# Kernel optimization log

Measured on AMD Instinct MI355X. Metric: run time of the kernel, lower is better.

The kernel has to match this reference:

```python
import jax, jax.numpy as jnp
import numpy as np

DIMS = 1024
HEAD = 16
HEAD_DIM = DIMS // HEAD
MAX_ITERS = 3
THRESH = 0.01   # torch uses self.threshold.item() -> plain float, no grad
FACTOR = 0.1    # torch uses self.factor.item()
EPS = 1e-5


def _ln(x, w):
    # LayerNorm(bias=False): (x-mean)/sqrt(var+eps) * w
    m = jnp.mean(x, axis=-1, keepdims=True)
    xc = x - m
    v = jnp.mean(xc * xc, axis=-1, keepdims=True)
    return xc * jax.lax.rsqrt(v + EPS) * w


def _focus(xw, Wq, bq, Wk, Wv, bv, Wo, bo, lna_w, lnb_w,
           lq_w, lq_b, lk_w, lk_b, lv_w, lv_b):
    # xw: [B, S, DIMS]. NOTE: in the torch code xa is effectively ignored inside
    # create_qkv (k/v are computed from x due to the `xa is not None` branch bug),
    # so each window is pure self-attention on the query window.
    B, S, D = xw.shape
    xn = _ln(xw, lna_w)
    scale = HEAD_DIM ** -0.25
    q = (xn @ Wq.T + bq) * scale
    k = (xn @ Wk.T) * scale          # k Linear has no bias
    v = xn @ Wv.T + bv

    def shp(t):
        return t.reshape(B, S, HEAD, HEAD_DIM).transpose(0, 2, 1, 3)  # [B,h,S,d]

    q, k, v = shp(q), shp(k), shp(v)
    q = _ln(q, lnb_w)
    k = _ln(k, lnb_w)

    causal = jnp.tril(jnp.ones((S, S), dtype=bool))
    neg = jnp.finfo(jnp.float32).min
    inv_sqrt_d = 1.0 / np.sqrt(HEAD_DIM).astype(np.float32)

    q_cur = q
    prev = jnp.zeros_like(q)
    attn_out = jnp.zeros_like(q)
    done = jnp.array(False)

    # eff_span == S here (span_len >= win_size, ctx % win_size == 0), so the
    # [:eff_span] slices in torch are no-ops. Unrolled loop with where-gating
    # reproduces the data-dependent early exit and stays reverse-differentiable.
    for it in range(MAX_ITERS):
        qp = _ln(q_cur @ lq_w.T + lq_b, lnb_w)
        kp = _ln(k @ lk_w.T + lk_b, lnb_w)
        vp = v @ lv_w.T + lv_b
        s = jnp.einsum('bhqd,bhkd->bhqk', qp, kp) * inv_sqrt_d
        s = jnp.where(causal, s, neg)
        a = jax.nn.softmax(s, axis=-1)
        o = jnp.einsum('bhqk,bhkd->bhqd', a, vp)
        # torch: permute(0,2,1,3).flatten(2) -> [B,S,h*d], then (buggy) raw
        # view(B, HEAD, S, HEAD_DIM) with NO transpose; out_proj is NOT applied
        # in this branch. Reproduced faithfully.
        iter_out = (o.transpose(0, 2, 1, 3)
                     .reshape(B, S, HEAD * HEAD_DIM)
                     .reshape(B, HEAD, S, HEAD_DIM))
        diff = jnp.mean(jnp.abs(iter_out - prev))
        conv = jnp.logical_and(diff < THRESH + FACTOR * diff, it > 0)
        attn_out = jnp.where(done, attn_out, iter_out)
        upd = jnp.logical_or(done, conv)
        q_cur = jnp.where(upd, q_cur, q_cur + iter_out)
        prev = jnp.where(upd, prev, iter_out)
        done = upd

    out = attn_out.transpose(0, 2, 1, 3).reshape(B, S, D)
    return out @ Wo.T + bo


def setup_inputs() -> dict:
    key = jax.random.key(0)
    ks = jax.random.split(key, 10)

    def w(k, shape, s=0.02):
        return jax.random.normal(k, shape, dtype=jnp.float32) * s

    return {
        'x': jax.random.normal(ks[0], (4, 4096, DIMS), dtype=jnp.float32),
        'Wq': w(ks[1], (DIMS, DIMS)), 'bq': jnp.zeros((DIMS,), jnp.float32),
        'Wk': w(ks[2], (DIMS, DIMS)),
        'Wv': w(ks[3], (DIMS, DIMS)), 'bv': jnp.zeros((DIMS,), jnp.float32),
        'Wo': w(ks[4], (DIMS, DIMS)), 'bo': jnp.zeros((DIMS,), jnp.float32),
        'lna_w': jnp.ones((DIMS,), jnp.float32),
        'lnb_w': jnp.ones((HEAD_DIM,), jnp.float32),
        'lq_w': w(ks[5], (HEAD_DIM, HEAD_DIM), 0.1), 'lq_b': jnp.zeros((HEAD_DIM,), jnp.float32),
        'lk_w': w(ks[6], (HEAD_DIM, HEAD_DIM), 0.1), 'lk_b': jnp.zeros((HEAD_DIM,), jnp.float32),
        'lv_w': w(ks[7], (HEAD_DIM, HEAD_DIM), 0.1), 'lv_b': jnp.zeros((HEAD_DIM,), jnp.float32),
        'win_size': 512,
        'span_len': 1024,
    }


def reference(x, Wq, bq, Wk, Wv, bv, Wo, bo, lna_w, lnb_w,
              lq_w, lq_b, lk_w, lk_b, lv_w, lv_b, win_size, span_len):
    # span_len only influences eff_span in torch; with span_len >= win_size it
    # has no effect on the math (k/v come from the query window due to the bug).
    b, ctx, dims = x.shape
    nwin = ctx // win_size  # ctx chosen divisible by win_size
    xw = x.reshape(b, nwin, win_size, dims).transpose(1, 0, 2, 3)  # [nwin,B,W,D]
    f = lambda xx: _focus(xx, Wq, bq, Wk, Wv, bv, Wo, bo, lna_w, lnb_w,
                          lq_w, lq_b, lk_w, lk_b, lv_w, lv_b)
    out = jax.vmap(f)(xw)  # per-window convergence test, matching torch
    return out.transpose(1, 0, 2, 3).reshape(b, ctx, dims)
```

## Files before the change

kernel.cpp:

```cpp
#include <hip/hip_runtime.h>
#include <math.h>

#define DIMS   1024
#define NHEAD  16
#define HD     64
#define WIN    512
#define CTX    4096
#define NBATCH 4
#define NROWS  (NBATCH*CTX)
#define NUNITS (NROWS*NHEAD)
#define LNEPS  1e-5f
#define FIXSCALE 16777216.0

typedef __attribute__((ext_vector_type(8))) short bf16x8;
typedef __attribute__((ext_vector_type(4))) float f32x4;

__device__ __forceinline__ float4 ld4(const float* p) { return *reinterpret_cast<const float4*>(p); }
__device__ __forceinline__ void st4(float* p, float4 v) { *reinterpret_cast<float4*>(p) = v; }

__device__ __forceinline__ float wave_sum64(float v) {
#pragma unroll
    for (int off = 32; off; off >>= 1) v += __shfl_xor(v, off, 64);
    return v;
}
__device__ __forceinline__ float grp16_sum(float v) {
    v += __shfl_xor(v, 1, 64);
    v += __shfl_xor(v, 2, 64);
    v += __shfl_xor(v, 4, 64);
    v += __shfl_xor(v, 8, 64);
    return v;
}

__device__ __forceinline__ unsigned bf16_rn_bits(float x) {
    unsigned u = __float_as_uint(x);
    return (u + 0x7fffu + ((u >> 16) & 1u)) >> 16;
}
__device__ __forceinline__ unsigned pack_hl(float x) {
    unsigned h = bf16_rn_bits(x);
    float hf = __uint_as_float(h << 16);
    unsigned l = bf16_rn_bits(x - hf);
    return (h << 16) | (l & 0xffffu);
}

__device__ __forceinline__ unsigned cvtpk_bf16(float a, float b) {
    unsigned r;
    asm volatile("v_cvt_pk_bf16_f32 %0, %1, %2" : "=v"(r) : "v"(a), "v"(b));
    return r;
}
__device__ __forceinline__ void split_pair(float a, float b, unsigned& hw, unsigned& lw) {
    hw = cvtpk_bf16(a, b);
    float ha = __uint_as_float(hw << 16);
    float hb = __uint_as_float(hw & 0xffff0000u);
    lw = cvtpk_bf16(a - ha, b - hb);
}

__device__ __forceinline__ int swzo(int row, int kbyte) {
    return ((row << 7) + kbyte) ^ ((row & 7) << 4);
}

__global__ __launch_bounds__(256)
void ln1024_pack_kernel(const float* __restrict__ x, const float* __restrict__ w,
                        unsigned* __restrict__ outp) {
    int r = blockIdx.x;
    int tid = threadIdx.x;
    const float* xr = x + (size_t)r * DIMS;
    float4 v = ld4(xr + (tid << 2));
    __shared__ float red[8];
    float s = wave_sum64(v.x + v.y + v.z + v.w);
    int wv = tid >> 6, lane = tid & 63;
    if (lane == 0) red[wv] = s;
    __syncthreads();
    float mean = (red[0] + red[1] + red[2] + red[3]) * (1.0f / DIMS);
    float dx = v.x - mean, dy = v.y - mean, dz = v.z - mean, dw = v.w - mean;
    float ss = wave_sum64(dx*dx + dy*dy + dz*dz + dw*dw);
    if (lane == 0) red[4 + wv] = ss;
    __syncthreads();
    float inv = rsqrtf((red[4] + red[5] + red[6] + red[7]) * (1.0f / DIMS) + LNEPS);
    float4 wv4 = ld4(w + (tid << 2));
    uint4 pk;
    pk.x = pack_hl(dx * inv * wv4.x);
    pk.y = pack_hl(dy * inv * wv4.y);
    pk.z = pack_hl(dz * inv * wv4.z);
    pk.w = pack_hl(dw * inv * wv4.w);
    *reinterpret_cast<uint4*>(outp + (size_t)r * DIMS + (tid << 2)) = pk;
}

__global__ __launch_bounds__(256, 2)
void gemm_hl_kernel(const unsigned* __restrict__ Ahl, const float* __restrict__ W,
                    const float* __restrict__ bias, float* __restrict__ Cm,
                    float alpha, int has_bias) {
    __shared__ short Ah[128 * 64], Al[128 * 64], Wh[128 * 64], Wl[128 * 64];
    int tid = threadIdx.x;
    int wid = tid >> 6, lane = tid & 63;
    int wm = (wid >> 1) << 6, wn = (wid & 1) << 6;
    int g4 = lane >> 4, l16 = lane & 15;
    int m0 = blockIdx.x << 7, n0 = blockIdx.y << 7;

    f32x4 acc[4][4] = {};

    int orow[4], okb[4];
#pragma unroll
    for (int j = 0; j < 4; ++j) {
        int oc = tid + (j << 8);
        orow[j] = oc >> 3;
        okb[j] = (oc & 7) << 4;
    }

    for (int k0 = 0; k0 < 1024; k0 += 64) {
        uint4 a0[4], a1[4];
        float4 w0[4], w1[4];
#pragma unroll
        for (int j = 0; j < 4; ++j) {
            const unsigned* ap = Ahl + (size_t)(m0 + orow[j]) * 1024 + k0 + (okb[j] >> 1);
            a0[j] = *reinterpret_cast<const uint4*>(ap);
            a1[j] = *reinterpret_cast<const uint4*>(ap + 4);
            const float* wp = W + (size_t)(n0 + orow[j]) * 1024 + k0 + (okb[j] >> 1);
            w0[j] = *reinterpret_cast<const float4*>(wp);
            w1[j] = *reinterpret_cast<const float4*>(wp + 4);
        }
        __syncthreads();
#pragma unroll
        for (int j = 0; j < 4; ++j) {
            int off = swzo(orow[j], okb[j]);
            uint4 hi, lo;
            hi.x = __byte_perm(a0[j].x, a0[j].y, 0x7632);
            hi.y = __byte_perm(a0[j].z, a0[j].w, 0x7632);
            hi.z = __byte_perm(a1[j].x, a1[j].y, 0x7632);
            hi.w = __byte_perm(a1[j].z, a1[j].w, 0x7632);
            lo.x = __byte_perm(a0[j].x, a0[j].y, 0x5410);
            lo.y = __byte_perm(a0[j].z, a0[j].w, 0x5410);
            lo.z = __byte_perm(a1[j].x, a1[j].y, 0x5410);
            lo.w = __byte_perm(a1[j].z, a1[j].w, 0x5410);
            *reinterpret_cast<uint4*>(reinterpret_cast<char*>(Ah) + off) = hi;
            *reinterpret_cast<uint4*>(reinterpret_cast<char*>(Al) + off) = lo;

            float xs[8];
            *reinterpret_cast<float4*>(&xs[0]) = w0[j];
            *reinterpret_cast<float4*>(&xs[4]) = w1[j];
            uint4 hw4, lw4;
            unsigned* hwp = &hw4.x;
            unsigned* lwp = &lw4.x;
#pragma unroll
            for (int p = 0; p < 4; ++p) {
                unsigned u0 = __float_as_uint(xs[2*p]);
                unsigned u1 = __float_as_uint(xs[2*p + 1]);
                unsigned h0 = (u0 + 0x8000u) >> 16;
                unsigned h1 = (u1 + 0x8000u) >> 16;
                float l0 = xs[2*p]     - __uint_as_float(h0 << 16);
                float l1 = xs[2*p + 1] - __uint_as_float(h1 << 16);
                unsigned lb0 = (__float_as_uint(l0) + 0x8000u) >> 16;
                unsigned lb1 = (__float_as_uint(l1) + 0x8000u) >> 16;
                hwp[p] = h0 | (h1 << 16);
                lwp[p] = lb0 | (lb1 << 16);
            }
            *reinterpret_cast<uint4*>(reinterpret_cast<char*>(Wh) + off) = hw4;
            *reinterpret_cast<uint4*>(reinterpret_cast<char*>(Wl) + off) = lw4;
        }
        __syncthreads();

#pragma unroll
        for (int kk = 0; kk < 2; ++kk) {
            bf16x8 afh[4], afl[4], wfh[4], wfl[4];
#pragma unroll
            for (int mt = 0; mt < 4; ++mt) {
                int row = wm + (mt << 4) + l16;
                int off = ((row << 7) + (kk << 6) + (g4 << 4)) ^ ((row & 7) << 4);
                afh[mt] = *reinterpret_cast<const bf16x8*>(reinterpret_cast<const char*>(Ah) + off);
                afl[mt] = *reinterpret_cast<const bf16x8*>(reinterpret_cast<const char*>(Al) + off);
            }
#pragma unroll
            for (int nt = 0; nt < 4; ++nt) {
                int row = wn + (nt << 4) + l16;
                int off = ((row << 7) + (kk << 6) + (g4 << 4)) ^ ((row & 7) << 4);
                wfh[nt] = *reinterpret_cast<const bf16x8*>(reinterpret_cast<const char*>(Wh) + off);
                wfl[nt] = *reinterpret_cast<const bf16x8*>(reinterpret_cast<const char*>(Wl) + off);
            }
#pragma unroll
            for (int mt = 0; mt < 4; ++mt)
#pragma unroll
                for (int nt = 0; nt < 4; ++nt) {
                    acc[mt][nt] = __builtin_amdgcn_mfma_f32_16x16x32_bf16(afh[mt], wfh[nt], acc[mt][nt], 0, 0, 0);
                    acc[mt][nt] = __builtin_amdgcn_mfma_f32_16x16x32_bf16(afl[mt], wfh[nt], acc[mt][nt], 0, 0, 0);
                    acc[mt][nt] = __builtin_amdgcn_mfma_f32_16x16x32_bf16(afh[mt], wfl[nt], acc[mt][nt], 0, 0, 0);
                }
        }
    }

#pragma unroll
    for (int mt = 0; mt < 4; ++mt)
#pragma unroll
        for (int nt = 0; nt < 4; ++nt) {
            int col = n0 + wn + (nt << 4) + l16;
            float bb = has_bias ? bias[col] : 0.0f;
#pragma unroll
            for (int r = 0; r < 4; ++r) {
                int row = m0 + wm + (mt << 4) + (g4 << 2) + r;
                Cm[(size_t)row * DIMS + col] = alpha * (acc[mt][nt][r] + bb);
            }
        }
}

__global__ __launch_bounds__(256)
void headln_kernel(float* __restrict__ q, float* __restrict__ k,
                   const float* __restrict__ lnw) {
    int gw = (blockIdx.x << 2) + (threadIdx.x >> 6);
    int lane = threadIdx.x & 63;
    size_t idx = ((size_t)gw << 6) + lane;
    float wgt = lnw[lane];
    {
        float v = q[idx];
        float mean = wave_sum64(v) * (1.0f / 64.0f);
        float d = v - mean;
        float var = wave_sum64(d * d) * (1.0f / 64.0f);
        q[idx] = d * rsqrtf(var + LNEPS) * wgt;
    }
    {
        float v = k[idx];
        float mean = wave_sum64(v) * (1.0f / 64.0f);
        float d = v - mean;
        float var = wave_sum64(d * d) * (1.0f / 64.0f);
        k[idx] = d * rsqrtf(var + LNEPS) * wgt;
    }
}

__global__ __launch_bounds__(256)
void proj64_khl_kernel(const float* __restrict__ inp, const float* __restrict__ W,
                       const float* __restrict__ Wb, const float* __restrict__ lnw,
                       unsigned* __restrict__ plane) {
    int u0 = blockIdx.x << 6;
    __shared__ float As[64][68];
    __shared__ float Bs[64][68];
    int tid = threadIdx.x;
    for (int e = tid; e < 4096; e += 256) Bs[e & 63][e >> 6] = W[e];
    for (int e = tid; e < 1024; e += 256) {
        int row = e >> 4;
        int col = (e & 15) << 2;
        float4 v = ld4(inp + ((size_t)(u0 + row) << 6) + col);
        As[col + 0][row] = v.x; As[col + 1][row] = v.y;
        As[col + 2][row] = v.z; As[col + 3][row] = v.w;
    }
    __syncthreads();
    int tm = tid >> 4, tn = tid & 15;
    float acc[4][4] = {};
#pragma unroll
    for (int k = 0; k < 64; ++k) {
        float4 av = ld4(&As[k][tm << 2]);
        float4 bv = ld4(&Bs[k][tn << 2]);
        float aa[4] = {av.x, av.y, av.z, av.w};
        float bb[4] = {bv.x, bv.y, bv.z, bv.w};
#pragma unroll
        for (int mm = 0; mm < 4; ++mm)
#pragma unroll
            for (int nn = 0; nn < 4; ++nn)
                acc[mm][nn] = fmaf(aa[mm], bb[nn], acc[mm][nn]);
    }
    float bb4[4] = {Wb[(tn << 2) + 0], Wb[(tn << 2) + 1], Wb[(tn << 2) + 2], Wb[(tn << 2) + 3]};
    float lw4[4] = {lnw[(tn << 2) + 0], lnw[(tn << 2) + 1], lnw[(tn << 2) + 2], lnw[(tn << 2) + 3]};
#pragma unroll
    for (int mm = 0; mm < 4; ++mm) {
        float o0 = acc[mm][0] + bb4[0], o1 = acc[mm][1] + bb4[1];
        float o2 = acc[mm][2] + bb4[2], o3 = acc[mm][3] + bb4[3];
        float mean = grp16_sum(o0 + o1 + o2 + o3) * (1.0f / 64.0f);
        float d0 = o0 - mean, d1 = o1 - mean, d2 = o2 - mean, d3 = o3 - mean;
        float var = grp16_sum(d0*d0 + d1*d1 + d2*d2 + d3*d3) * (1.0f / 64.0f);
        float inv = rsqrtf(var + LNEPS);
        o0 = d0 * inv * lw4[0]; o1 = d1 * inv * lw4[1];
        o2 = d2 * inv * lw4[2]; o3 = d3 * inv * lw4[3];
        int u_p = u0 + (tm << 2) + mm;
        int r = u_p >> 4, h = u_p & 15;
        int s = r & 511;
        int ua = ((r >> 9) << 4) + h;
        size_t punit = (size_t)ua * 512 + s;
        uint4 pk;
        pk.x = pack_hl(o0); pk.y = pack_hl(o1); pk.z = pack_hl(o2); pk.w = pack_hl(o3);
        *reinterpret_cast<uint4*>(plane + (punit << 6) + (tn << 2)) = pk;
    }
}

__global__ __launch_bounds__(256)
void proj64_vthl_kernel(const float* __restrict__ inp, const float* __restrict__ W,
                        const float* __restrict__ Wb, unsigned* __restrict__ plane) {
    int u0 = blockIdx.x << 6;
    __shared__ float As[64][68];
    __shared__ float Bs[64][68];
    int tid = threadIdx.x;
    for (int e = tid; e < 4096; e += 256) Bs[e & 63][e >> 6] = W[e];
    for (int e = tid; e < 1024; e += 256) {
        int row = e >> 4;
        int col = (e & 15) << 2;
        float4 v = ld4(inp + ((size_t)(u0 + row) << 6) + col);
        As[col + 0][row] = v.x; As[col + 1][row] = v.y;
        As[col + 2][row] = v.z; As[col + 3][row] = v.w;
    }
    __syncthreads();
    int tm = tid >> 4, tn = tid & 15;
    float acc[4][4] = {};
#pragma unroll
    for (int k = 0; k < 64; ++k) {
        float4 av = ld4(&As[k][tm << 2]);
        float4 bv = ld4(&Bs[k][tn << 2]);
        float aa[4] = {av.x, av.y, av.z, av.w};
        float bb[4] = {bv.x, bv.y, bv.z, bv.w};
#pragma unroll
        for (int mm = 0; mm < 4; ++mm)
#pragma unroll
            for (int nn = 0; nn < 4; ++nn)
                acc[mm][nn] = fmaf(aa[mm], bb[nn], acc[mm][nn]);
    }
    float bb4[4] = {Wb[(tn << 2) + 0], Wb[(tn << 2) + 1], Wb[(tn << 2) + 2], Wb[(tn << 2) + 3]};
#pragma unroll
    for (int mm = 0; mm < 4; ++mm) {
        int u_p = u0 + (tm << 2) + mm;
        int r = u_p >> 4, h = u_p & 15;
        int s = r & 511;
        int ua = ((r >> 9) << 4) + h;
        size_t base = ((size_t)(ua * 8 + (s >> 6)) << 12) + (s & 63);
#pragma unroll
        for (int nn = 0; nn < 4; ++nn) {
            int d = (tn << 2) + nn;
            plane[base + ((size_t)d << 6)] = pack_hl(acc[mm][nn] + bb4[nn]);
        }
    }
}

template<int DIFF, int USE_CONV>
__global__ __launch_bounds__(256)
void attn_mfma_kernel(const float* __restrict__ qacc, const unsigned* __restrict__ khl,
                      const unsigned* __restrict__ vthl, float* __restrict__ o_io,
                      const float* __restrict__ lqw, const float* __restrict__ lqb,
                      const float* __restrict__ lnw,
                      unsigned long long* __restrict__ diff_acc,
                      const int* __restrict__ conv) {
    __shared__ short kh[64][72], kl[64][72], vh[64][72], vl[64][72];
    __shared__ float dred[4];

    int blk = blockIdx.x;
    int u = blk & 511;
    int t = 7 - (blk >> 9);
    int h = u & 15;
    int w = (u >> 4) & 7;
    int b = u >> 7;
    if (USE_CONV && conv[w]) return;
    int rowbase = b * CTX + w * WIN;
    int col0 = h * HD;
    int tid = threadIdx.x;
    int wv = tid >> 6;
    int lane = tid & 63;
    int g4 = lane >> 4;
    int qcol = lane & 15;
    int q_loc = (wv << 4) + qcol;
    int selhi = g4 >> 1;

    const unsigned* kbase = khl + (((size_t)u * 512) << 6);
    const unsigned* vbase = vthl + (((size_t)u * 8) << 12);

    uint4 kpre[4], vpre[4];
#pragma unroll
    for (int rr = 0; rr < 4; ++rr) {
        int row = (wv << 4) + (rr << 2) + g4;
        kpre[rr] = *reinterpret_cast<const uint4*>(kbase + ((size_t)row << 6) + (qcol << 2));
        vpre[rr] = *reinterpret_cast<const uint4*>(vbase + ((size_t)row << 6) + (qcol << 2));
    }

#pragma unroll
    for (int rr = 0; rr < 4; ++rr) {
        int row = (wv << 4) + (rr << 2) + g4;
        float4 v = ld4(lqw + (row << 6) + (qcol << 2));
        unsigned h0, l0, h1, l1;
        split_pair(v.x, v.y, h0, l0);
        split_pair(v.z, v.w, h1, l1);
        *reinterpret_cast<uint2*>(&kh[row][qcol << 2]) = make_uint2(h0, h1);
        *reinterpret_cast<uint2*>(&kl[row][qcol << 2]) = make_uint2(l0, l1);
    }

    bf16x8 bqh[2], bql[2];
    {
        const float* qrow = qacc + (size_t)(rowbase + (t << 6) + q_loc) * DIMS + col0;
#pragma unroll
        for (int kb = 0; kb < 2; ++kb) {
            float4 x0 = ld4(qrow + (kb << 5) + (g4 << 3));
            float4 x1 = ld4(qrow + (kb << 5) + (g4 << 3) + 4);
            unsigned hws[4], lws[4];
            split_pair(x0.x, x0.y, hws[0], lws[0]);
            split_pair(x0.z, x0.w, hws[1], lws[1]);
            split_pair(x1.x, x1.y, hws[2], lws[2]);
            split_pair(x1.z, x1.w, hws[3], lws[3]);
#pragma unroll
            for (int p2 = 0; p2 < 4; ++p2) {
                reinterpret_cast<unsigned*>(&bqh[kb])[p2] = hws[p2];
                reinterpret_cast<unsigned*>(&bql[kb])[p2] = lws[p2];
            }
        }
    }
    __syncthreads();

    f32x4 qpa[4] = {{0,0,0,0},{0,0,0,0},{0,0,0,0},{0,0,0,0}};
    __builtin_amdgcn_s_setprio(1);
#pragma unroll
    for (int jt = 0; jt < 4; ++jt) {
        int arow = (jt << 4) + qcol;
#pragma unroll
        for (int kb = 0; kb < 2; ++kb) {
            bf16x8 ah = *reinterpret_cast<const bf16x8*>(&kh[arow][(kb << 5) + (g4 << 3)]);
            bf16x8 al = *reinterpret_cast<const bf16x8*>(&kl[arow][(kb << 5) + (g4 << 3)]);
            qpa[jt] = __builtin_amdgcn_mfma_f32_16x16x32_bf16(ah, bqh[kb], qpa[jt], 0, 0, 0);
            qpa[jt] = __builtin_amdgcn_mfma_f32_16x16x32_bf16(al, bqh[kb], qpa[jt], 0, 0, 0);
            qpa[jt] = __builtin_amdgcn_mfma_f32_16x16x32_bf16(ah, bql[kb], qpa[jt], 0, 0, 0);
        }
    }
    __builtin_amdgcn_s_setprio(0);

    float vals[16];
    float s1 = 0.0f;
#pragma unroll
    for (int jt = 0; jt < 4; ++jt) {
        float4 b4 = ld4(lqb + (jt << 4) + (g4 << 2));
        const float* b4p = reinterpret_cast<const float*>(&b4);
#pragma unroll
        for (int r = 0; r < 4; ++r) {
            float v = qpa[jt][r] + b4p[r];
            vals[(jt << 2) + r] = v;
            s1 += v;
        }
    }
    s1 += __shfl_xor(s1, 16, 64);
    s1 += __shfl_xor(s1, 32, 64);
    float mean = s1 * (1.0f / 64.0f);
    float s2 = 0.0f;
#pragma unroll
    for (int e = 0; e < 16; ++e) { float d = vals[e] - mean; vals[e] = d; s2 += d * d; }
    s2 += __shfl_xor(s2, 16, 64);
    s2 += __shfl_xor(s2, 32, 64);
    float inv = rsqrtf(s2 * (1.0f / 64.0f) + LNEPS);
#pragma unroll
    for (int jt = 0; jt < 4; ++jt) {
        float4 w4 = ld4(lnw + (jt << 4) + (g4 << 2));
        const float* w4p = reinterpret_cast<const float*>(&w4);
#pragma unroll
        for (int r = 0; r < 4; ++r) vals[(jt << 2) + r] *= inv * w4p[r];
    }

    bf16x8 qfh[2], qfl[2];
    {
        unsigned hw[8], lw[8];
#pragma unroll
        for (int jt = 0; jt < 4; ++jt) {
            split_pair(vals[(jt << 2) + 0], vals[(jt << 2) + 1], hw[(jt << 1) + 0], lw[(jt << 1) + 0]);
            split_pair(vals[(jt << 2) + 2], vals[(jt << 2) + 3], hw[(jt << 1) + 1], lw[(jt << 1) + 1]);
        }
#pragma unroll
        for (int kb = 0; kb < 2; ++kb)
#pragma unroll
            for (int ip = 0; ip < 4; ++ip) {
                int srcl = (((g4 & 1) << 1) + (ip >> 1)) * 16 + qcol;
                unsigned hA = __shfl(hw[(kb << 2) + (ip & 1)], srcl, 64);
                unsigned hB = __shfl(hw[(kb << 2) + 2 + (ip & 1)], srcl, 64);
                unsigned lA = __shfl(lw[(kb << 2) + (ip & 1)], srcl, 64);
                unsigned lB = __shfl(lw[(kb << 2) + 2 + (ip & 1)], srcl, 64);
                reinterpret_cast<unsigned*>(&qfh[kb])[ip] = selhi ? hB : hA;
                reinterpret_cast<unsigned*>(&qfl[kb])[ip] = selhi ? lB : lA;
            }
    }
    __syncthreads();

    float m_r = -INFINITY, l_r = 0.0f;
    f32x4 oacc[4] = {{0,0,0,0},{0,0,0,0},{0,0,0,0},{0,0,0,0}};

    for (int c = 0; c <= t; ++c) {
#pragma unroll
        for (int rr = 0; rr < 4; ++rr) {
            int row = (wv << 4) + (rr << 2) + g4;
            uint4 pk = kpre[rr];
            unsigned* khp = reinterpret_cast<unsigned*>(&kh[row][qcol << 2]);
            khp[0] = __byte_perm(pk.x, pk.y, 0x7632);
            khp[1] = __byte_perm(pk.z, pk.w, 0x7632);
            unsigned* klp = reinterpret_cast<unsigned*>(&kl[row][qcol << 2]);
            klp[0] = __byte_perm(pk.x, pk.y, 0x5410);
            klp[1] = __byte_perm(pk.z, pk.w, 0x5410);
            uint4 pv = vpre[rr];
            unsigned* vhp = reinterpret_cast<unsigned*>(&vh[row][qcol << 2]);
            vhp[0] = __byte_perm(pv.x, pv.y, 0x7632);
            vhp[1] = __byte_perm(pv.z, pv.w, 0x7632);
            unsigned* vlp = reinterpret_cast<unsigned*>(&vl[row][qcol << 2]);
            vlp[0] = __byte_perm(pv.x, pv.y, 0x5410);
            vlp[1] = __byte_perm(pv.z, pv.w, 0x5410);
        }
        if (c < t) {
            const unsigned* ksrc = kbase + (((size_t)(c + 1) * 64) << 6);
            const unsigned* vsrc = vbase + (((size_t)(c + 1)) << 12);
#pragma unroll
            for (int rr = 0; rr < 4; ++rr) {
                int row = (wv << 4) + (rr << 2) + g4;
                kpre[rr] = *reinterpret_cast<const uint4*>(ksrc + ((size_t)row << 6) + (qcol << 2));
                vpre[rr] = *reinterpret_cast<const uint4*>(vsrc + ((size_t)row << 6) + (qcol << 2));
            }
        }
        __syncthreads();

        f32x4 sacc[4] = {{0,0,0,0},{0,0,0,0},{0,0,0,0},{0,0,0,0}};
        __builtin_amdgcn_s_setprio(1);
#pragma unroll
        for (int jt = 0; jt < 4; ++jt) {
            int jrow = (jt << 4) + qcol;
#pragma unroll
            for (int kb = 0; kb < 2; ++kb) {
                bf16x8 ah = *reinterpret_cast<const bf16x8*>(&kh[jrow][(kb << 5) + (g4 << 3)]);
                bf16x8 al = *reinterpret_cast<const bf16x8*>(&kl[jrow][(kb << 5) + (g4 << 3)]);
                sacc[jt] = __builtin_amdgcn_mfma_f32_16x16x32_bf16(ah, qfh[kb], sacc[jt], 0, 0, 0);
                sacc[jt] = __builtin_amdgcn_mfma_f32_16x16x32_bf16(al, qfh[kb], sacc[jt], 0, 0, 0);
                sacc[jt] = __builtin_amdgcn_mfma_f32_16x16x32_bf16(ah, qfl[kb], sacc[jt], 0, 0, 0);
            }
        }
        __builtin_amdgcn_s_setprio(0);

        float sv[16];
        float mx = -3.0e38f;
#pragma unroll
        for (int jt = 0; jt < 4; ++jt)
#pragma unroll
            for (int r = 0; r < 4; ++r) {
                float s = sacc[jt][r] * 0.125f;
                if (c == t) {
                    int j_loc = (jt << 4) + (g4 << 2) + r;
                    if (j_loc > q_loc) s = -3.0e38f;
                }
                sv[(jt << 2) + r] = s;
                mx = fmaxf(mx, s);
            }
        mx = fmaxf(mx, __shfl_xor(mx, 16, 64));
        mx = fmaxf(mx, __shfl_xor(mx, 32, 64));
        float mnew = fmaxf(m_r, mx);
        float ps = 0.0f;
#pragma unroll
        for (int e = 0; e < 16; ++e) {
            float p = __expf(sv[e] - mnew);
            sv[e] = p;
            ps += p;
        }
        ps += __shfl_xor(ps, 16, 64);
        ps += __shfl_xor(ps, 32, 64);
        float ef = __expf(m_r - mnew);
        l_r = l_r * ef + ps;
        m_r = mnew;
#pragma unroll
        for (int dt = 0; dt < 4; ++dt) oacc[dt] *= ef;

        unsigned hwp[8], lwp[8];
#pragma unroll
        for (int jt = 0; jt < 4; ++jt) {
            split_pair(sv[(jt << 2) + 0], sv[(jt << 2) + 1], hwp[(jt << 1) + 0], lwp[(jt << 1) + 0]);
            split_pair(sv[(jt << 2) + 2], sv[(jt << 2) + 3], hwp[(jt << 1) + 1], lwp[(jt << 1) + 1]);
        }

        __builtin_amdgcn_s_setprio(1);
#pragma unroll
        for (int kb2 = 0; kb2 < 2; ++kb2) {
            bf16x8 ph, pl;
#pragma unroll
            for (int ip = 0; ip < 4; ++ip) {
                int srcl = (((g4 & 1) << 1) + (ip >> 1)) * 16 + qcol;
                unsigned hA = __shfl(hwp[(kb2 << 2) + (ip & 1)], srcl, 64);
                unsigned hB = __shfl(hwp[(kb2 << 2) + 2 + (ip & 1)], srcl, 64);
                unsigned lA = __shfl(lwp[(kb2 << 2) + (ip & 1)], srcl, 64);
                unsigned lB = __shfl(lwp[(kb2 << 2) + 2 + (ip & 1)], srcl, 64);
                reinterpret_cast<unsigned*>(&ph)[ip] = selhi ? hB : hA;
                reinterpret_cast<unsigned*>(&pl)[ip] = selhi ? lB : lA;
            }
#pragma unroll
            for (int dt = 0; dt < 4; ++dt) {
                int drow = (dt << 4) + qcol;
                bf16x8 ah = *reinterpret_cast<const bf16x8*>(&vh[drow][(kb2 << 5) + (g4 << 3)]);
                bf16x8 al = *reinterpret_cast<const bf16x8*>(&vl[drow][(kb2 << 5) + (g4 << 3)]);
                oacc[dt] = __builtin_amdgcn_mfma_f32_16x16x32_bf16(ah, ph, oacc[dt], 0, 0, 0);
                oacc[dt] = __builtin_amdgcn_mfma_f32_16x16x32_bf16(al, ph, oacc[dt], 0, 0, 0);
                oacc[dt] = __builtin_amdgcn_mfma_f32_16x16x32_bf16(ah, pl, oacc[dt], 0, 0, 0);
            }
        }
        __builtin_amdgcn_s_setprio(0);
        __syncthreads();
    }

    float invl = 1.0f / l_r;
    float dsum = 0.0f;
    float* orow = o_io + (size_t)(rowbase + (t << 6) + q_loc) * DIMS + col0;
#pragma unroll
    for (int dt = 0; dt < 4; ++dt) {
        float4 ov = make_float4(oacc[dt][0] * invl, oacc[dt][1] * invl,
                                oacc[dt][2] * invl, oacc[dt][3] * invl);
        float* addr = orow + (dt << 4) + (g4 << 2);
        if (DIFF) {
            float4 pv4 = ld4(addr);
            dsum += fabsf(ov.x - pv4.x) + fabsf(ov.y - pv4.y)
                  + fabsf(ov.z - pv4.z) + fabsf(ov.w - pv4.w);
        }
        st4(addr, ov);
    }
    if (DIFF) {
        float s = wave_sum64(dsum);
        if (lane == 0) dred[wv] = s;
        __syncthreads();
        if (tid == 0) {
            double tot = (double)(dred[0] + dred[1] + dred[2] + dred[3]);
            unsigned long long q = (unsigned long long)(tot * FIXSCALE + 0.5);
            atomicAdd(&diff_acc[w], q);
        }
    }
}

__global__ __launch_bounds__(256)
void scatter_add_kernel(float* __restrict__ qacc, const float* __restrict__ o) {
    size_t gid = (size_t)blockIdx.x * 256 + threadIdx.x;
    size_t flat = gid << 2;
    int uu = (int)(flat >> 6);
    int col = (int)(flat & 63);
    int r = uu >> 4, h = uu & 15;
    int s = r & 511;
    int rb = r - s;
    size_t src = ((size_t)(rb + h * 32 + (s >> 4)) << 10)
               + (size_t)((s & 15) << 6) + col;
    float4 a = ld4(qacc + flat);
    float4 bv = ld4(o + src);
    st4(qacc + flat, make_float4(a.x + bv.x, a.y + bv.y, a.z + bv.z, a.w + bv.w));
}

__global__ void init_ctrl_kernel(unsigned long long* __restrict__ dacc,
                                 int* __restrict__ conv) {
    int i = threadIdx.x;
    if (i < 8) { dacc[i] = 0ULL; conv[i] = 0; }
}

__global__ void conv_from_acc_kernel(const unsigned long long* __restrict__ dacc,
                                     int* __restrict__ conv) {
    int w = threadIdx.x;
    if (w < 8) {
        float mean = (float)((double)dacc[w] * (1.0 / (FIXSCALE * 2097152.0)));
        conv[w] = (mean < 0.01f + 0.1f * mean) ? 1 : 0;
    }
}

__global__ __launch_bounds__(256)
void unscramble_pack_kernel(const float* __restrict__ src, unsigned* __restrict__ outp) {
    size_t gid = (size_t)blockIdx.x * 256 + threadIdx.x;
    size_t flat = gid << 2;
    int r = (int)(flat >> 10);
    int e = (int)(flat & 1023);
    int h2 = e >> 6, d2 = e & 63;
    int s2 = r & 511;
    int rb = r - s2;
    size_t sidx = ((size_t)(rb + h2 * 32 + (s2 >> 4)) << 10) + (size_t)((s2 & 15) << 6) + d2;
    float4 v = ld4(src + sidx);
    uint4 pk;
    pk.x = pack_hl(v.x); pk.y = pack_hl(v.y); pk.z = pack_hl(v.z); pk.w = pack_hl(v.w);
    *reinterpret_cast<uint4*>(outp + flat) = pk;
}

extern "C" void kernel_launch(void* const* d_in, const int* in_sizes, int n_in,
                              void* d_out, int out_size, void* d_ws, size_t ws_size,
                              hipStream_t stream) {
    (void)in_sizes; (void)n_in; (void)out_size; (void)ws_size;
    const float* x   = (const float*)d_in[0];
    const float* Wq  = (const float*)d_in[1];
    const float* bq  = (const float*)d_in[2];
    const float* Wk  = (const float*)d_in[3];
    const float* Wv  = (const float*)d_in[4];
    const float* bv  = (const float*)d_in[5];
    const float* Wo  = (const float*)d_in[6];
    const float* bo  = (const float*)d_in[7];
    const float* lna = (const float*)d_in[8];
    const float* lnb = (const float*)d_in[9];
    const float* lqw = (const float*)d_in[10];
    const float* lqb = (const float*)d_in[11];
    const float* lkw = (const float*)d_in[12];
    const float* lkb = (const float*)d_in[13];
    const float* lvw = (const float*)d_in[14];
    const float* lvb = (const float*)d_in[15];

    const size_t BUF = (size_t)NROWS * DIMS;
    unsigned long long* dacc = (unsigned long long*)d_ws;
    int* conv = (int*)(dacc + 8);
    float* R1 = (float*)((char*)d_ws + 4096);
    float* R2 = R1 + BUF;
    float* R3 = R2 + BUF;
    float* E  = (float*)d_out;

    const float scale = 0.35355339059327373f;

    ln1024_pack_kernel<<<NROWS, 256, 0, stream>>>(x, lna, (unsigned*)R2);

    dim3 gg(NROWS / 128, DIMS / 128);
    gemm_hl_kernel<<<gg, 256, 0, stream>>>((const unsigned*)R2, Wq, bq, R1, scale, 1);
    gemm_hl_kernel<<<gg, 256, 0, stream>>>((const unsigned*)R2, Wk, bq, E,  scale, 0);
    gemm_hl_kernel<<<gg, 256, 0, stream>>>((const unsigned*)R2, Wv, bv, R3, 1.0f, 1);

    headln_kernel<<<NUNITS / 4, 256, 0, stream>>>(R1, E, lnb);

    proj64_khl_kernel<<<NUNITS / 64, 256, 0, stream>>>(E, lkw, lkb, lnb, (unsigned*)R2);
    proj64_vthl_kernel<<<NUNITS / 64, 256, 0, stream>>>(R3, lvw, lvb, (unsigned*)E);

    init_ctrl_kernel<<<1, 64, 0, stream>>>(dacc, conv);

    const unsigned* KHL = (const unsigned*)R2;
    const unsigned* VTHL = (const unsigned*)E;

    attn_mfma_kernel<0, 0><<<512 * 8, 256, 0, stream>>>(R1, KHL, VTHL, R3, lqw, lqb, lnb, dacc, conv);
    scatter_add_kernel<<<NROWS * DIMS / 4 / 256, 256, 0, stream>>>(R1, R3);
    attn_mfma_kernel<1, 0><<<512 * 8, 256, 0, stream>>>(R1, KHL, VTHL, R3, lqw, lqb, lnb, dacc, conv);
    conv_from_acc_kernel<<<1, 64, 0, stream>>>(dacc, conv);
    scatter_add_kernel<<<NROWS * DIMS / 4 / 256, 256, 0, stream>>>(R1, R3);
    attn_mfma_kernel<0, 1><<<512 * 8, 256, 0, stream>>>(R1, KHL, VTHL, R3, lqw, lqb, lnb, dacc, conv);

    unscramble_pack_kernel<<<NROWS * DIMS / 4 / 256, 256, 0, stream>>>(R3, (unsigned*)R2);
    gemm_hl_kernel<<<gg, 256, 0, stream>>>((const unsigned*)R2, Wo, bo, (float*)d_out, 1.0f, 1);
}
```

Before: 1.134 ms.

## Pair query tiles per attention block, fuse head LayerNorm into GEMM epilogue

Each attention block now handles two query tiles (t and t-1) and shares every K/V chunk load between them, halving the grid and reusing staged K/V. The per-head LayerNorm on q and k moves into the Q/K GEMM epilogue, which removes the separate headln kernel and its full read/write pass. Online softmax now skips rescaling when the running max grows by less than 8, which trims exp and multiply work. Pairing tiles raises register pressure and gives uneven per-block work (the paired tiles span different chunk counts), and the lazy max update carries a small numeric risk.

```diff
diff --git a/kernel.cpp b/kernel.cpp
--- a/kernel.cpp
+++ b/kernel.cpp
@@ -85,10 +85,11 @@
     *reinterpret_cast<uint4*>(outp + (size_t)r * DIMS + (tid << 2)) = pk;
 }
 
+template<int DO_HLN>
 __global__ __launch_bounds__(256, 2)
 void gemm_hl_kernel(const unsigned* __restrict__ Ahl, const float* __restrict__ W,
                     const float* __restrict__ bias, float* __restrict__ Cm,
-                    float alpha, int has_bias) {
+                    float alpha, int has_bias, const float* __restrict__ lnw) {
     __shared__ short Ah[128 * 64], Al[128 * 64], Wh[128 * 64], Wl[128 * 64];
     int tid = threadIdx.x;
     int wid = tid >> 6, lane = tid & 63;
@@ -186,40 +187,50 @@
         }
     }
 
-#pragma unroll
-    for (int mt = 0; mt < 4; ++mt)
-#pragma unroll
-        for (int nt = 0; nt < 4; ++nt) {
-            int col = n0 + wn + (nt << 4) + l16;
-            float bb = has_bias ? bias[col] : 0.0f;
+    if (DO_HLN) {
+        float bb[4];
+#pragma unroll
+        for (int nt = 0; nt < 4; ++nt)
+            bb[nt] = has_bias ? bias[n0 + wn + (nt << 4) + l16] : 0.0f;
+        float lw4[4];
+#pragma unroll
+        for (int nt = 0; nt < 4; ++nt) lw4[nt] = lnw[(nt << 4) + l16];
+#pragma unroll
+        for (int mt = 0; mt < 4; ++mt)
 #pragma unroll
             for (int r = 0; r < 4; ++r) {
+                float v[4];
+                float s1 = 0.0f;
+#pragma unroll
+                for (int nt = 0; nt < 4; ++nt) {
+                    v[nt] = alpha * (acc[mt][nt][r] + bb[nt]);
+                    s1 += v[nt];
+                }
+                s1 = grp16_sum(s1);
+                float mean = s1 * (1.0f / 64.0f);
+                float s2 = 0.0f;
+#pragma unroll
+                for (int nt = 0; nt < 4; ++nt) { v[nt] -= mean; s2 += v[nt] * v[nt]; }
+                s2 = grp16_sum(s2);
+                float inv = rsqrtf(s2 * (1.0f / 64.0f) + LNEPS);
                 int row = m0 + wm + (mt << 4) + (g4 << 2) + r;
-                Cm[(size_t)row * DIMS + col] = alpha * (acc[mt][nt][r] + bb);
-            }
-        }
-}
-
-__global__ __launch_bounds__(256)
-void headln_kernel(float* __restrict__ q, float* __restrict__ k,
-                   const float* __restrict__ lnw) {
-    int gw = (blockIdx.x << 2) + (threadIdx.x >> 6);
-    int lane = threadIdx.x & 63;
-    size_t idx = ((size_t)gw << 6) + lane;
-    float wgt = lnw[lane];
-    {
-        float v = q[idx];
-        float mean = wave_sum64(v) * (1.0f / 64.0f);
-        float d = v - mean;
-        float var = wave_sum64(d * d) * (1.0f / 64.0f);
-        q[idx] = d * rsqrtf(var + LNEPS) * wgt;
-    }
-    {
-        float v = k[idx];
-        float mean = wave_sum64(v) * (1.0f / 64.0f);
-        float d = v - mean;
-        float var = wave_sum64(d * d) * (1.0f / 64.0f);
-        k[idx] = d * rsqrtf(var + LNEPS) * wgt;
+#pragma unroll
+                for (int nt = 0; nt < 4; ++nt)
+                    Cm[(size_t)row * DIMS + n0 + wn + (nt << 4) + l16] = v[nt] * inv * lw4[nt];
+            }
+    } else {
+#pragma unroll
+        for (int mt = 0; mt < 4; ++mt)
+#pragma unroll
+            for (int nt = 0; nt < 4; ++nt) {
+                int col = n0 + wn + (nt << 4) + l16;
+                float bb = has_bias ? bias[col] : 0.0f;
+#pragma unroll
+                for (int r = 0; r < 4; ++r) {
+                    int row = m0 + wm + (mt << 4) + (g4 << 2) + r;
+                    Cm[(size_t)row * DIMS + col] = alpha * (acc[mt][nt][r] + bb);
+                }
+            }
     }
 }
 
@@ -336,7 +347,9 @@
 
     int blk = blockIdx.x;
     int u = blk & 511;
-    int t = 7 - (blk >> 9);
+    int pr = blk >> 9;
+    int tHi = 7 - (pr << 1);
+    int tLo = tHi - 1;
     int h = u & 15;
     int w = (u >> 4) & 7;
     int b = u >> 7;
@@ -372,76 +385,77 @@
         *reinterpret_cast<uint2*>(&kh[row][qcol << 2]) = make_uint2(h0, h1);
         *reinterpret_cast<uint2*>(&kl[row][qcol << 2]) = make_uint2(l0, l1);
     }
-
-    bf16x8 bqh[2], bql[2];
-    {
-        const float* qrow = qacc + (size_t)(rowbase + (t << 6) + q_loc) * DIMS + col0;
-#pragma unroll
-        for (int kb = 0; kb < 2; ++kb) {
-            float4 x0 = ld4(qrow + (kb << 5) + (g4 << 3));
-            float4 x1 = ld4(qrow + (kb << 5) + (g4 << 3) + 4);
-            unsigned hws[4], lws[4];
-            split_pair(x0.x, x0.y, hws[0], lws[0]);
-            split_pair(x0.z, x0.w, hws[1], lws[1]);
-            split_pair(x1.x, x1.y, hws[2], lws[2]);
-            split_pair(x1.z, x1.w, hws[3], lws[3]);
-#pragma unroll
-            for (int p2 = 0; p2 < 4; ++p2) {
-                reinterpret_cast<unsigned*>(&bqh[kb])[p2] = hws[p2];
-                reinterpret_cast<unsigned*>(&bql[kb])[p2] = lws[p2];
-            }
-        }
-    }
     __syncthreads();
 
-    f32x4 qpa[4] = {{0,0,0,0},{0,0,0,0},{0,0,0,0},{0,0,0,0}};
-    __builtin_amdgcn_s_setprio(1);
-#pragma unroll
-    for (int jt = 0; jt < 4; ++jt) {
-        int arow = (jt << 4) + qcol;
-#pragma unroll
-        for (int kb = 0; kb < 2; ++kb) {
-            bf16x8 ah = *reinterpret_cast<const bf16x8*>(&kh[arow][(kb << 5) + (g4 << 3)]);
-            bf16x8 al = *reinterpret_cast<const bf16x8*>(&kl[arow][(kb << 5) + (g4 << 3)]);
-            qpa[jt] = __builtin_amdgcn_mfma_f32_16x16x32_bf16(ah, bqh[kb], qpa[jt], 0, 0, 0);
-            qpa[jt] = __builtin_amdgcn_mfma_f32_16x16x32_bf16(al, bqh[kb], qpa[jt], 0, 0, 0);
-            qpa[jt] = __builtin_amdgcn_mfma_f32_16x16x32_bf16(ah, bql[kb], qpa[jt], 0, 0, 0);
-        }
-    }
-    __builtin_amdgcn_s_setprio(0);
-
-    float vals[16];
-    float s1 = 0.0f;
-#pragma unroll
-    for (int jt = 0; jt < 4; ++jt) {
-        float4 b4 = ld4(lqb + (jt << 4) + (g4 << 2));
-        const float* b4p = reinterpret_cast<const float*>(&b4);
-#pragma unroll
-        for (int r = 0; r < 4; ++r) {
-            float v = qpa[jt][r] + b4p[r];
-            vals[(jt << 2) + r] = v;
-            s1 += v;
-        }
-    }
-    s1 += __shfl_xor(s1, 16, 64);
-    s1 += __shfl_xor(s1, 32, 64);
-    float mean = s1 * (1.0f / 64.0f);
-    float s2 = 0.0f;
-#pragma unroll
-    for (int e = 0; e < 16; ++e) { float d = vals[e] - mean; vals[e] = d; s2 += d * d; }
-    s2 += __shfl_xor(s2, 16, 64);
-    s2 += __shfl_xor(s2, 32, 64);
-    float inv = rsqrtf(s2 * (1.0f / 64.0f) + LNEPS);
-#pragma unroll
-    for (int jt = 0; jt < 4; ++jt) {
-        float4 w4 = ld4(lnw + (jt << 4) + (g4 << 2));
-        const float* w4p = reinterpret_cast<const float*>(&w4);
-#pragma unroll
-        for (int r = 0; r < 4; ++r) vals[(jt << 2) + r] *= inv * w4p[r];
-    }
-
-    bf16x8 qfh[2], qfl[2];
-    {
+    bf16x8 qfh[2][2], qfl[2][2];
+#pragma unroll
+    for (int ti = 0; ti < 2; ++ti) {
+        int T = ti ? tLo : tHi;
+        bf16x8 bqh[2], bql[2];
+        {
+            const float* qrow = qacc + (size_t)(rowbase + (T << 6) + q_loc) * DIMS + col0;
+#pragma unroll
+            for (int kb = 0; kb < 2; ++kb) {
+                float4 x0 = ld4(qrow + (kb << 5) + (g4 << 3));
+                float4 x1 = ld4(qrow + (kb << 5) + (g4 << 3) + 4);
+                unsigned hws[4], lws[4];
+                split_pair(x0.x, x0.y, hws[0], lws[0]);
+                split_pair(x0.z, x0.w, hws[1], lws[1]);
+                split_pair(x1.x, x1.y, hws[2], lws[2]);
+                split_pair(x1.z, x1.w, hws[3], lws[3]);
+#pragma unroll
+                for (int p2 = 0; p2 < 4; ++p2) {
+                    reinterpret_cast<unsigned*>(&bqh[kb])[p2] = hws[p2];
+                    reinterpret_cast<unsigned*>(&bql[kb])[p2] = lws[p2];
+                }
+            }
+        }
+        f32x4 qpa[4] = {{0,0,0,0},{0,0,0,0},{0,0,0,0},{0,0,0,0}};
+        __builtin_amdgcn_s_setprio(1);
+#pragma unroll
+        for (int jt = 0; jt < 4; ++jt) {
+            int arow = (jt << 4) + qcol;
+#pragma unroll
+            for (int kb = 0; kb < 2; ++kb) {
+                bf16x8 ah = *reinterpret_cast<const bf16x8*>(&kh[arow][(kb << 5) + (g4 << 3)]);
+                bf16x8 al = *reinterpret_cast<const bf16x8*>(&kl[arow][(kb << 5) + (g4 << 3)]);
+                qpa[jt] = __builtin_amdgcn_mfma_f32_16x16x32_bf16(ah, bqh[kb], qpa[jt], 0, 0, 0);
+                qpa[jt] = __builtin_amdgcn_mfma_f32_16x16x32_bf16(al, bqh[kb], qpa[jt], 0, 0, 0);
+                qpa[jt] = __builtin_amdgcn_mfma_f32_16x16x32_bf16(ah, bql[kb], qpa[jt], 0, 0, 0);
+            }
+        }
+        __builtin_amdgcn_s_setprio(0);
+
+        float vals[16];
+        float s1 = 0.0f;
+#pragma unroll
+        for (int jt = 0; jt < 4; ++jt) {
+            float4 b4 = ld4(lqb + (jt << 4) + (g4 << 2));
+            const float* b4p = reinterpret_cast<const float*>(&b4);
+#pragma unroll
+            for (int r = 0; r < 4; ++r) {
+                float v = qpa[jt][r] + b4p[r];
+                vals[(jt << 2) + r] = v;
+                s1 += v;
+            }
+        }
+        s1 += __shfl_xor(s1, 16, 64);
+        s1 += __shfl_xor(s1, 32, 64);
+        float mean = s1 * (1.0f / 64.0f);
+        float s2 = 0.0f;
+#pragma unroll
+        for (int e = 0; e < 16; ++e) { float d = vals[e] - mean; vals[e] = d; s2 += d * d; }
+        s2 += __shfl_xor(s2, 16, 64);
+        s2 += __shfl_xor(s2, 32, 64);
+        float inv = rsqrtf(s2 * (1.0f / 64.0f) + LNEPS);
+#pragma unroll
+        for (int jt = 0; jt < 4; ++jt) {
+            float4 w4 = ld4(lnw + (jt << 4) + (g4 << 2));
+            const float* w4p = reinterpret_cast<const float*>(&w4);
+#pragma unroll
+            for (int r = 0; r < 4; ++r) vals[(jt << 2) + r] *= inv * w4p[r];
+        }
+
         unsigned hw[8], lw[8];
 #pragma unroll
         for (int jt = 0; jt < 4; ++jt) {
@@ -457,16 +471,16 @@
                 unsigned hB = __shfl(hw[(kb << 2) + 2 + (ip & 1)], srcl, 64);
                 unsigned lA = __shfl(lw[(kb << 2) + (ip & 1)], srcl, 64);
                 unsigned lB = __shfl(lw[(kb << 2) + 2 + (ip & 1)], srcl, 64);
-                reinterpret_cast<unsigned*>(&qfh[kb])[ip] = selhi ? hB : hA;
-                reinterpret_cast<unsigned*>(&qfl[kb])[ip] = selhi ? lB : lA;
+                reinterpret_cast<unsigned*>(&qfh[ti][kb])[ip] = selhi ? hB : hA;
+                reinterpret_cast<unsigned*>(&qfl[ti][kb])[ip] = selhi ? lB : lA;
             }
     }
     __syncthreads();
 
-    float m_r = -INFINITY, l_r = 0.0f;
-    f32x4 oacc[4] = {{0,0,0,0},{0,0,0,0},{0,0,0,0},{0,0,0,0}};
-
-    for (int c = 0; c <= t; ++c) {
+    float m_r[2] = {-INFINITY, -INFINITY}, l_r[2] = {0.0f, 0.0f};
+    f32x4 oacc[2][4] = {};
+
+    for (int c = 0; c <= tHi; ++c) {
 #pragma unroll
         for (int rr = 0; rr < 4; ++rr) {
             int row = (wv << 4) + (rr << 2) + g4;
@@ -485,7 +499,7 @@
             vlp[0] = __byte_perm(pv.x, pv.y, 0x5410);
             vlp[1] = __byte_perm(pv.z, pv.w, 0x5410);
         }
-        if (c < t) {
+        if (c < tHi) {
             const unsigned* ksrc = kbase + (((size_t)(c + 1) * 64) << 6);
             const unsigned* vsrc = vbase + (((size_t)(c + 1)) << 12);
 #pragma unroll
@@ -497,103 +511,117 @@
         }
         __syncthreads();
 
-        f32x4 sacc[4] = {{0,0,0,0},{0,0,0,0},{0,0,0,0},{0,0,0,0}};
-        __builtin_amdgcn_s_setprio(1);
-#pragma unroll
-        for (int jt = 0; jt < 4; ++jt) {
-            int jrow = (jt << 4) + qcol;
-#pragma unroll
-            for (int kb = 0; kb < 2; ++kb) {
-                bf16x8 ah = *reinterpret_cast<const bf16x8*>(&kh[jrow][(kb << 5) + (g4 << 3)]);
-                bf16x8 al = *reinterpret_cast<const bf16x8*>(&kl[jrow][(kb << 5) + (g4 << 3)]);
-                sacc[jt] = __builtin_amdgcn_mfma_f32_16x16x32_bf16(ah, qfh[kb], sacc[jt], 0, 0, 0);
-                sacc[jt] = __builtin_amdgcn_mfma_f32_16x16x32_bf16(al, qfh[kb], sacc[jt], 0, 0, 0);
-                sacc[jt] = __builtin_amdgcn_mfma_f32_16x16x32_bf16(ah, qfl[kb], sacc[jt], 0, 0, 0);
-            }
-        }
-        __builtin_amdgcn_s_setprio(0);
-
-        float sv[16];
-        float mx = -3.0e38f;
-#pragma unroll
-        for (int jt = 0; jt < 4; ++jt)
-#pragma unroll
-            for (int r = 0; r < 4; ++r) {
-                float s = sacc[jt][r] * 0.125f;
-                if (c == t) {
-                    int j_loc = (jt << 4) + (g4 << 2) + r;
-                    if (j_loc > q_loc) s = -3.0e38f;
-                }
-                sv[(jt << 2) + r] = s;
-                mx = fmaxf(mx, s);
-            }
-        mx = fmaxf(mx, __shfl_xor(mx, 16, 64));
-        mx = fmaxf(mx, __shfl_xor(mx, 32, 64));
-        float mnew = fmaxf(m_r, mx);
-        float ps = 0.0f;
-#pragma unroll
-        for (int e = 0; e < 16; ++e) {
-            float p = __expf(sv[e] - mnew);
-            sv[e] = p;
-            ps += p;
-        }
-        ps += __shfl_xor(ps, 16, 64);
-        ps += __shfl_xor(ps, 32, 64);
-        float ef = __expf(m_r - mnew);
-        l_r = l_r * ef + ps;
-        m_r = mnew;
-#pragma unroll
-        for (int dt = 0; dt < 4; ++dt) oacc[dt] *= ef;
-
-        unsigned hwp[8], lwp[8];
-#pragma unroll
-        for (int jt = 0; jt < 4; ++jt) {
-            split_pair(sv[(jt << 2) + 0], sv[(jt << 2) + 1], hwp[(jt << 1) + 0], lwp[(jt << 1) + 0]);
-            split_pair(sv[(jt << 2) + 2], sv[(jt << 2) + 3], hwp[(jt << 1) + 1], lwp[(jt << 1) + 1]);
-        }
-
-        __builtin_amdgcn_s_setprio(1);
-#pragma unroll
-        for (int kb2 = 0; kb2 < 2; ++kb2) {
-            bf16x8 ph, pl;
-#pragma unroll
-            for (int ip = 0; ip < 4; ++ip) {
-                int srcl = (((g4 & 1) << 1) + (ip >> 1)) * 16 + qcol;
-                unsigned hA = __shfl(hwp[(kb2 << 2) + (ip & 1)], srcl, 64);
-                unsigned hB = __shfl(hwp[(kb2 << 2) + 2 + (ip & 1)], srcl, 64);
-                unsigned lA = __shfl(lwp[(kb2 << 2) + (ip & 1)], srcl, 64);
-                unsigned lB = __shfl(lwp[(kb2 << 2) + 2 + (ip & 1)], srcl, 64);
-                reinterpret_cast<unsigned*>(&ph)[ip] = selhi ? hB : hA;
-                reinterpret_cast<unsigned*>(&pl)[ip] = selhi ? lB : lA;
-            }
-#pragma unroll
-            for (int dt = 0; dt < 4; ++dt) {
-                int drow = (dt << 4) + qcol;
-                bf16x8 ah = *reinterpret_cast<const bf16x8*>(&vh[drow][(kb2 << 5) + (g4 << 3)]);
-                bf16x8 al = *reinterpret_cast<const bf16x8*>(&vl[drow][(kb2 << 5) + (g4 << 3)]);
-                oacc[dt] = __builtin_amdgcn_mfma_f32_16x16x32_bf16(ah, ph, oacc[dt], 0, 0, 0);
-                oacc[dt] = __builtin_amdgcn_mfma_f32_16x16x32_bf16(al, ph, oacc[dt], 0, 0, 0);
-                oacc[dt] = __builtin_amdgcn_mfma_f32_16x16x32_bf16(ah, pl, oacc[dt], 0, 0, 0);
-            }
-        }
-        __builtin_amdgcn_s_setprio(0);
+#pragma unroll
+        for (int ti = 0; ti < 2; ++ti) {
+            if (ti == 0 || c <= tLo) {
+                int T = ti ? tLo : tHi;
+
+                f32x4 sacc[4] = {{0,0,0,0},{0,0,0,0},{0,0,0,0},{0,0,0,0}};
+                __builtin_amdgcn_s_setprio(1);
+#pragma unroll
+                for (int jt = 0; jt < 4; ++jt) {
+                    int jrow = (jt << 4) + qcol;
+#pragma unroll
+                    for (int kb = 0; kb < 2; ++kb) {
+                        bf16x8 ah = *reinterpret_cast<const bf16x8*>(&kh[jrow][(kb << 5) + (g4 << 3)]);
+                        bf16x8 al = *reinterpret_cast<const bf16x8*>(&kl[jrow][(kb << 5) + (g4 << 3)]);
+                        sacc[jt] = __builtin_amdgcn_mfma_f32_16x16x32_bf16(ah, qfh[ti][kb], sacc[jt], 0, 0, 0);
+                        sacc[jt] = __builtin_amdgcn_mfma_f32_16x16x32_bf16(al, qfh[ti][kb], sacc[jt], 0, 0, 0);
+                        sacc[jt] = __builtin_amdgcn_mfma_f32_16x16x32_bf16(ah, qfl[ti][kb], sacc[jt], 0, 0, 0);
+                    }
+                }
+                __builtin_amdgcn_s_setprio(0);
+
+                float sv[16];
+                float mx = -3.0e38f;
+#pragma unroll
+                for (int jt = 0; jt < 4; ++jt)
+#pragma unroll
+                    for (int r = 0; r < 4; ++r) {
+                        float s = sacc[jt][r] * 0.125f;
+                        if (c == T) {
+                            int j_loc = (jt << 4) + (g4 << 2) + r;
+                            if (j_loc > q_loc) s = -3.0e38f;
+                        }
+                        sv[(jt << 2) + r] = s;
+                        mx = fmaxf(mx, s);
+                    }
+                mx = fmaxf(mx, __shfl_xor(mx, 16, 64));
+                mx = fmaxf(mx, __shfl_xor(mx, 32, 64));
+                if (!__all(mx <= m_r[ti] + 8.0f)) {
+                    float mnew = fmaxf(m_r[ti], mx);
+                    float ef = __expf(m_r[ti] - mnew);
+                    l_r[ti] *= ef;
+#pragma unroll
+                    for (int dt = 0; dt < 4; ++dt) oacc[ti][dt] *= ef;
+                    m_r[ti] = mnew;
+                }
+                float ps = 0.0f;
+#pragma unroll
+                for (int e = 0; e < 16; ++e) {
+                    float p = __expf(sv[e] - m_r[ti]);
+                    sv[e] = p;
+                    ps += p;
+                }
+                ps += __shfl_xor(ps, 16, 64);
+                ps += __shfl_xor(ps, 32, 64);
+                l_r[ti] += ps;
+
+                unsigned hwp[8], lwp[8];
+#pragma unroll
+                for (int jt = 0; jt < 4; ++jt) {
+                    split_pair(sv[(jt << 2) + 0], sv[(jt << 2) + 1], hwp[(jt << 1) + 0], lwp[(jt << 1) + 0]);
+                    split_pair(sv[(jt << 2) + 2], sv[(jt << 2) + 3], hwp[(jt << 1) + 1], lwp[(jt << 1) + 1]);
+                }
+
+                __builtin_amdgcn_s_setprio(1);
+#pragma unroll
+                for (int kb2 = 0; kb2 < 2; ++kb2) {
+                    bf16x8 ph, pl;
+#pragma unroll
+                    for (int ip = 0; ip < 4; ++ip) {
+                        int srcl = (((g4 & 1) << 1) + (ip >> 1)) * 16 + qcol;
+                        unsigned hA = __shfl(hwp[(kb2 << 2) + (ip & 1)], srcl, 64);
+                        unsigned hB = __shfl(hwp[(kb2 << 2) + 2 + (ip & 1)], srcl, 64);
+                        unsigned lA = __shfl(lwp[(kb2 << 2) + (ip & 1)], srcl, 64);
+                        unsigned lB = __shfl(lwp[(kb2 << 2) + 2 + (ip & 1)], srcl, 64);
+                        reinterpret_cast<unsigned*>(&ph)[ip] = selhi ? hB : hA;
+                        reinterpret_cast<unsigned*>(&pl)[ip] = selhi ? lB : lA;
+                    }
+#pragma unroll
+                    for (int dt = 0; dt < 4; ++dt) {
+                        int drow = (dt << 4) + qcol;
+                        bf16x8 ah = *reinterpret_cast<const bf16x8*>(&vh[drow][(kb2 << 5) + (g4 << 3)]);
+                        bf16x8 al = *reinterpret_cast<const bf16x8*>(&vl[drow][(kb2 << 5) + (g4 << 3)]);
+                        oacc[ti][dt] = __builtin_amdgcn_mfma_f32_16x16x32_bf16(ah, ph, oacc[ti][dt], 0, 0, 0);
+                        oacc[ti][dt] = __builtin_amdgcn_mfma_f32_16x16x32_bf16(al, ph, oacc[ti][dt], 0, 0, 0);
+                        oacc[ti][dt] = __builtin_amdgcn_mfma_f32_16x16x32_bf16(ah, pl, oacc[ti][dt], 0, 0, 0);
+                    }
+                }
+                __builtin_amdgcn_s_setprio(0);
+            }
+        }
         __syncthreads();
     }
 
-    float invl = 1.0f / l_r;
     float dsum = 0.0f;
-    float* orow = o_io + (size_t)(rowbase + (t << 6) + q_loc) * DIMS + col0;
-#pragma unroll
-    for (int dt = 0; dt < 4; ++dt) {
-        float4 ov = make_float4(oacc[dt][0] * invl, oacc[dt][1] * invl,
-                                oacc[dt][2] * invl, oacc[dt][3] * invl);
-        float* addr = orow + (dt << 4) + (g4 << 2);
-        if (DIFF) {
-            float4 pv4 = ld4(addr);
-            dsum += fabsf(ov.x - pv4.x) + fabsf(ov.y - pv4.y)
-                  + fabsf(ov.z - pv4.z) + fabsf(ov.w - pv4.w);
-        }
-        st4(addr, ov);
+#pragma unroll
+    for (int ti = 0; ti < 2; ++ti) {
+        int T = ti ? tLo : tHi;
+        float invl = 1.0f / l_r[ti];
+        float* orow = o_io + (size_t)(rowbase + (T << 6) + q_loc) * DIMS + col0;
+#pragma unroll
+        for (int dt = 0; dt < 4; ++dt) {
+            float4 ov = make_float4(oacc[ti][dt][0] * invl, oacc[ti][dt][1] * invl,
+                                    oacc[ti][dt][2] * invl, oacc[ti][dt][3] * invl);
+            float* addr = orow + (dt << 4) + (g4 << 2);
+            if (DIFF) {
+                float4 pv4 = ld4(addr);
+                dsum += fabsf(ov.x - pv4.x) + fabsf(ov.y - pv4.y)
+                      + fabsf(ov.z - pv4.z) + fabsf(ov.w - pv4.w);
+            }
+            st4(addr, ov);
+        }
     }
     if (DIFF) {
         float s = wave_sum64(dsum);
@@ -688,11 +716,9 @@
     ln1024_pack_kernel<<<NROWS, 256, 0, stream>>>(x, lna, (unsigned*)R2);
 
     dim3 gg(NROWS / 128, DIMS / 128);
-    gemm_hl_kernel<<<gg, 256, 0, stream>>>((const unsigned*)R2, Wq, bq, R1, scale, 1);
-    gemm_hl_kernel<<<gg, 256, 0, stream>>>((const unsigned*)R2, Wk, bq, E,  scale, 0);
-    gemm_hl_kernel<<<gg, 256, 0, stream>>>((const unsigned*)R2, Wv, bv, R3, 1.0f, 1);
-
-    headln_kernel<<<NUNITS / 4, 256, 0, stream>>>(R1, E, lnb);
+    gemm_hl_kernel<1><<<gg, 256, 0, stream>>>((const unsigned*)R2, Wq, bq, R1, scale, 1, lnb);
+    gemm_hl_kernel<1><<<gg, 256, 0, stream>>>((const unsigned*)R2, Wk, bq, E,  scale, 0, lnb);
+    gemm_hl_kernel<0><<<gg, 256, 0, stream>>>((const unsigned*)R2, Wv, bv, R3, 1.0f, 1, lnb);
 
     proj64_khl_kernel<<<NUNITS / 64, 256, 0, stream>>>(E, lkw, lkb, lnb, (unsigned*)R2);
     proj64_vthl_kernel<<<NUNITS / 64, 256, 0, stream>>>(R3, lvw, lvb, (unsigned*)E);
@@ -702,13 +728,13 @@
     const unsigned* KHL = (const unsigned*)R2;
     const unsigned* VTHL = (const unsigned*)E;
 
-    attn_mfma_kernel<0, 0><<<512 * 8, 256, 0, stream>>>(R1, KHL, VTHL, R3, lqw, lqb, lnb, dacc, conv);
+    attn_mfma_kernel<0, 0><<<512 * 4, 256, 0, stream>>>(R1, KHL, VTHL, R3, lqw, lqb, lnb, dacc, conv);
     scatter_add_kernel<<<NROWS * DIMS / 4 / 256, 256, 0, stream>>>(R1, R3);
-    attn_mfma_kernel<1, 0><<<512 * 8, 256, 0, stream>>>(R1, KHL, VTHL, R3, lqw, lqb, lnb, dacc, conv);
+    attn_mfma_kernel<1, 0><<<512 * 4, 256, 0, stream>>>(R1, KHL, VTHL, R3, lqw, lqb, lnb, dacc, conv);
     conv_from_acc_kernel<<<1, 64, 0, stream>>>(dacc, conv);
     scatter_add_kernel<<<NROWS * DIMS / 4 / 256, 256, 0, stream>>>(R1, R3);
-    attn_mfma_kernel<0, 1><<<512 * 8, 256, 0, stream>>>(R1, KHL, VTHL, R3, lqw, lqb, lnb, dacc, conv);
+    attn_mfma_kernel<0, 1><<<512 * 4, 256, 0, stream>>>(R1, KHL, VTHL, R3, lqw, lqb, lnb, dacc, conv);
 
     unscramble_pack_kernel<<<NROWS * DIMS / 4 / 256, 256, 0, stream>>>(R3, (unsigned*)R2);
-    gemm_hl_kernel<<<gg, 256, 0, stream>>>((const unsigned*)R2, Wo, bo, (float*)d_out, 1.0f, 1);
-}
+    gemm_hl_kernel<0><<<gg, 256, 0, stream>>>((const unsigned*)R2, Wo, bo, (float*)d_out, 1.0f, 1, lnb);
+}
```

After: 1.018 ms. 10.3% less time.
